# Kernel tuning notes

Hardware: AMD Instinct MI355X
Metric: run time of the kernel (lower is better)

The kernel has to match this reference:

```python
import jax, jax.numpy as jnp
import numpy as np

PHI = (1.0 + 5.0 ** 0.5) / 2.0
TWO_PI = 2.0 * np.pi
LN_EPS = 1e-5


def _complex_linear(xr, xi, Wr, Wi, br, bi):
    # (Wr + i*Wi) @ (xr + i*xi) + (br + i*bi)
    yr = xr @ Wr.T - xi @ Wi.T + br
    yi = xr @ Wi.T + xi @ Wr.T + bi
    return yr, yi


def _layernorm(x, g, b):
    m = jnp.mean(x, axis=-1, keepdims=True)
    v = jnp.mean((x - m) ** 2, axis=-1, keepdims=True)
    return (x - m) * jax.lax.rsqrt(v + LN_EPS) * g + b


def reference(w, b, ip_Wr, ip_Wi, ip_br, ip_bi, ln_g, ln_b, W_qkv, log_alpha, op_Wr, op_Wi):
    B, S, D = w.shape
    H = log_alpha.shape[0]
    Dh = D // H
    scale = jnp.sqrt(jnp.asarray(Dh, w.dtype))
    alpha = jax.nn.sigmoid(log_alpha)[None, :, None]  # (1,H,1)
    ts = jnp.arange(S, dtype=w.dtype)

    def step(carry, xs):
        hr, hi, vs = carry          # (B,D),(B,D),(B,H,Dh)
        w_t, b_t, t = xs            # (B,D),(B,D),()
        # InstrumentedEulerTransform: separated theta, complex product
        wl = 1.0 + jnp.abs(w_t)
        tphi = (t * PHI) % TWO_PI   # wrap_time_periodic
        thr = hr / wl + b_t + tphi
        thi = hi / wl + b_t + tphi
        sr, cr = jnp.sin(thr), jnp.cos(thr)
        si, ci = jnp.sin(thi), jnp.cos(thi)
        hr2 = cr * ci - sr * si
        hi2 = cr * si + sr * ci
        # InstrumentedEchoChamber.forward_step
        pr, pi_ = _complex_linear(hr2, hi2, ip_Wr, ip_Wi, ip_br, ip_bi)
        xc = _layernorm(pr + pi_, ln_g, ln_b)
        qkv = (xc @ W_qkv.T).reshape(B, 3, H, Dh)
        q, k, v = qkv[:, 0], qkv[:, 1], qkv[:, 2]
        vs2 = alpha * v + (1.0 - alpha) * vs
        gate = jax.nn.sigmoid(jnp.sum(q * k, axis=-1, keepdims=True) / scale)
        retr = (gate * vs2).reshape(B, D)
        # output_proj ComplexLinear on (retr, 0), no bias
        ore = retr @ op_Wr.T
        oim = retr @ op_Wi.T
        return (hr2, hi2, vs2), (ore, oim)

    init = (jnp.zeros((B, D), w.dtype), jnp.zeros((B, D), w.dtype),
            jnp.zeros((B, H, Dh), w.dtype))
    wT = jnp.swapaxes(w, 0, 1)  # (S,B,D)
    bT = jnp.swapaxes(b, 0, 1)
    _, (or_seq, oi_seq) = jax.lax.scan(step, init, (wT, bT, ts))
    out = jnp.stack([or_seq, oi_seq])      # (2,S,B,D)
    return jnp.swapaxes(out, 1, 2)         # (2,B,S,D)


def setup_inputs() -> dict:
    key = jax.random.key(0)
    ks = jax.random.split(key, 10)
    B, S, D, H = 8, 2048, 512, 8
    s = 0.02
    return {
        "w": jax.random.normal(ks[0], (B, S, D), jnp.float32),
        "b": jax.random.normal(ks[1], (B, S, D), jnp.float32),
        "ip_Wr": jax.random.normal(ks[2], (D, D), jnp.float32) * s,
        "ip_Wi": jax.random.normal(ks[3], (D, D), jnp.float32) * s,
        "ip_br": jax.random.normal(ks[4], (D,), jnp.float32) * s,
        "ip_bi": jax.random.normal(ks[5], (D,), jnp.float32) * s,
        "ln_g": jnp.ones((D,), jnp.float32),
        "ln_b": jnp.zeros((D,), jnp.float32),
        "W_qkv": jax.random.normal(ks[6], (3 * D, D), jnp.float32) * s,
        "log_alpha": jax.random.normal(ks[7], (H,), jnp.float32),
        "op_Wr": jax.random.normal(ks[8], (D, D), jnp.float32) * s,
        "op_Wi": jax.random.normal(ks[9], (D, D), jnp.float32) * s,
    }
```

## Files before the change

kernel.cpp:

```cpp
#include <hip/hip_runtime.h>
#include <math.h>

#define BB 8
#define SS 2048
#define DD 512
#define HH 8
#define MM (BB*SS)

#define CHK 128
#define CL  16
#define CW  48

#define RT 32
#define RW 128

typedef unsigned short u16;
typedef unsigned int   u32;
typedef float f32x4 __attribute__((ext_vector_type(4)));
typedef short s16x8 __attribute__((ext_vector_type(8)));

__device__ __forceinline__ u16 f2bf(float x){
  union { float f; unsigned u; } c; c.f = x;
  unsigned r = c.u + 0x7FFF + ((c.u >> 16) & 1);
  return (u16)(r >> 16);
}
__device__ __forceinline__ float bf2f(u16 x){
  union { unsigned u; float f; } c; c.u = ((unsigned)x) << 16;
  return c.f;
}
__device__ __forceinline__ void gload16(const u16* g, u16* l){
  __builtin_amdgcn_global_load_lds(
      (const __attribute__((address_space(1))) unsigned int*)g,
      (__attribute__((address_space(3))) unsigned int*)l, 16, 0, 0);
}

__global__ void prep_all(const float* __restrict__ ipWr, const float* __restrict__ ipWi,
                         const float* __restrict__ Wqkv,
                         const float* __restrict__ opWr, const float* __restrict__ opWi,
                         const float* __restrict__ ipbr, const float* __restrict__ ipbi,
                         const float* __restrict__ la,
                         u16* __restrict__ W1, u16* __restrict__ Wq, u16* __restrict__ W3,
                         float* __restrict__ tphi2, float* __restrict__ bc,
                         float* __restrict__ alph){
  int id = blockIdx.x*256 + threadIdx.x;
  if (id < 524288){
    int n = id >> 10, k = id & 1023;
    int d = k >> 1;
    float v = (k & 1) ? (ipWr[n*512+d] - ipWi[n*512+d])
                      : (ipWr[n*512+d] + ipWi[n*512+d]);
    W1[id] = f2bf(v);
  } else if (id < 1310720){
    int i = id - 524288;
    Wq[i] = f2bf(Wqkv[i]);
  } else if (id < 1835008){
    int i = id - 1310720;
    int n = i >> 9, k = i & 511;
    W3[i] = f2bf((n < 512) ? opWr[n*512+k] : opWi[(n-512)*512+k]);
  } else if (id < 1837056){
    int t = id - 1835008;
    const float PHI_F    = 1.61803398874989484820f;
    const float TWO_PI_F = 6.28318530717958647693f;
    tphi2[t] = 2.0f * fmodf((float)t * PHI_F, TWO_PI_F);
  } else if (id < 1837568){
    int t = id - 1837056;
    bc[t] = ipbr[t] + ipbi[t];
  } else if (id < 1837576){
    int t = id - 1837568;
    alph[t] = 1.0f/(1.0f + expf(-la[t]));
  }
}

__global__ __launch_bounds__(256) void scan_h(const float* __restrict__ w,
                                              const float* __restrict__ bb,
                                              const float* __restrict__ tphi2,
                                              u32* __restrict__ X32){
  const int e = blockIdx.x*256 + threadIdx.x;
  const int c = blockIdx.y;
  const int b = e >> 9;
  const int d = e & 511;
  const float SQRT2 = 1.41421356237309504880f;
  const float PI_4  = 0.78539816339744830962f;
  const int tstart = c*CL;
  int t0 = tstart - CW; if (t0 < 0) t0 = 0;
  const int nw = tstart - t0;

  const float* wp = w  + ((size_t)b*SS + t0)*DD + d;
  const float* bp = bb + ((size_t)b*SS + t0)*DD + d;
  const float* tp = tphi2 + t0;

  const int U = 8;
  float wv[U], bv[U], wn[U], bn[U];

  float ss = 0.f;
  const int ngw = nw >> 3;
  if (ngw > 0){
    #pragma unroll
    for (int i=0;i<U;i++){ wv[i] = wp[(size_t)i*DD]; bv[i] = bp[(size_t)i*DD]; }
    for (int gg=0; gg<ngw; ++gg){
      if (gg+1 < ngw){
        const float* wnp = wp + (size_t)(gg+1)*U*DD;
        const float* bnp = bp + (size_t)(gg+1)*U*DD;
        #pragma unroll
        for (int i=0;i<U;i++){ wn[i] = wnp[(size_t)i*DD]; bn[i] = bnp[(size_t)i*DD]; }
      }
      #pragma unroll
      for (int i=0;i<U;i++){
        float rwl2 = SQRT2 * __builtin_amdgcn_rcpf(1.0f + fabsf(wv[i]));
        float cw   = fmaf(2.0f, bv[i], tp[gg*U+i]) + PI_4;
        ss = __sinf(fmaf(ss, rwl2, cw));
      }
      #pragma unroll
      for (int i=0;i<U;i++){ wv[i]=wn[i]; bv[i]=bn[i]; }
    }
  }
  float hs = SQRT2 * ss;

  const float* wq = wp + (size_t)nw*DD;
  const float* bq = bp + (size_t)nw*DD;
  const float* tq = tp + nw;
  u32* xp = X32 + (size_t)(b*SS + tstart)*512 + d;

  #pragma unroll
  for (int i=0;i<U;i++){ wv[i] = wq[(size_t)i*DD]; bv[i] = bq[(size_t)i*DD]; }
  for (int gg=0; gg<CL/U; ++gg){
    if (gg+1 < CL/U){
      const float* wnp = wq + (size_t)(gg+1)*U*DD;
      const float* bnp = bq + (size_t)(gg+1)*U*DD;
      #pragma unroll
      for (int i=0;i<U;i++){ wn[i] = wnp[(size_t)i*DD]; bn[i] = bnp[(size_t)i*DD]; }
    }
    #pragma unroll
    for (int i=0;i<U;i++){
      float rwl = __builtin_amdgcn_rcpf(1.0f + fabsf(wv[i]));
      float cc  = fmaf(2.0f, bv[i], tq[gg*U+i]);
      float theta = fmaf(hs, rwl, cc);
      float sn = __sinf(theta);
      float cs = __cosf(theta);
      hs = cs + sn;
      xp[(size_t)(gg*U+i)*512] = (u32)f2bf(cs) | ((u32)f2bf(sn) << 16);
    }
    #pragma unroll
    for (int i=0;i<U;i++){ wv[i]=wn[i]; bv[i]=bn[i]; }
  }
}

template<int TAG, int EPI>
__global__ __launch_bounds__(256) void gemm_bf16(const u16* __restrict__ A,
                                                 const u16* __restrict__ W,
                                                 float* __restrict__ C0,
                                                 float* __restrict__ C1,
                                                 u16* __restrict__ C2,
                                                 int N, int K){
  __shared__ __align__(16) u16 As[3][128*32];
  __shared__ __align__(16) u16 Bs[3][128*32];
  const int tid  = threadIdx.x;
  const int nwgx = gridDim.x;
  const int nwg  = nwgx * gridDim.y;
  const int lin  = blockIdx.y * nwgx + blockIdx.x;
  const int qq   = nwg >> 3;
  const int logi = (lin & 7) * qq + (lin >> 3);
  const int m0   = (logi / nwgx) * 128;
  const int n0   = (logi % nwgx) * 128;

  const int wave = tid >> 6;
  const int lane = tid & 63;
  const int wr   = wave >> 1, wc = wave & 1;
  const int l15  = lane & 15;
  const int g    = lane >> 4;

  const int rI   = lane >> 2;
  const int kgs  = (lane & 3) ^ ((lane >> 3) & 3);
  const int row0 = (wave*2+0)*16 + rI;
  const int row1 = (wave*2+1)*16 + rI;
  const u16* Asrc0 = A + (size_t)(m0 + row0) * K + kgs*8;
  const u16* Asrc1 = A + (size_t)(m0 + row1) * K + kgs*8;
  const u16* Bsrc0 = W + (size_t)(n0 + row0) * K + kgs*8;
  const u16* Bsrc1 = W + (size_t)(n0 + row1) * K + kgs*8;
  const int ld0 = (wave*2+0)*512;
  const int ld1 = (wave*2+1)*512;

  f32x4 acc[4][4];
  #pragma unroll
  for (int i=0;i<4;i++)
    #pragma unroll
    for (int j=0;j<4;j++) acc[i][j] = (f32x4){0.f,0.f,0.f,0.f};

#define STAGE(buf, koff) do {                      \
    gload16(Asrc0 + (koff), &As[buf][ld0]);        \
    gload16(Asrc1 + (koff), &As[buf][ld1]);        \
    gload16(Bsrc0 + (koff), &Bs[buf][ld0]);        \
    gload16(Bsrc1 + (koff), &Bs[buf][ld1]);        \
  } while(0)

#define COMPUTE(buf) do {                                            \
    s16x8 af[4], bf[4];                                              \
    _Pragma("unroll")                                                \
    for (int s=0;s<4;s++){                                           \
      int rA = wr*64 + s*16 + l15;                                   \
      af[s] = *(const s16x8*)&As[buf][rA*32 + ((g ^ ((rA>>1)&3))*8)];\
      int rB = wc*64 + s*16 + l15;                                   \
      bf[s] = *(const s16x8*)&Bs[buf][rB*32 + ((g ^ ((rB>>1)&3))*8)];\
    }                                                                \
    _Pragma("unroll")                                                \
    for (int mi=0;mi<4;mi++)                                         \
      _Pragma("unroll")                                              \
      for (int ni=0;ni<4;ni++)                                       \
        acc[mi][ni] = __builtin_amdgcn_mfma_f32_16x16x32_bf16(af[mi], bf[ni], acc[mi][ni], 0, 0, 0); \
  } while(0)

  const int nt = K >> 5;
  STAGE(0, 0);
  STAGE(1, 32);
  int cur = 0;
  for (int t = 0; t < nt; ++t){
    if (t+2 < nt){
      int nb = cur+2; if (nb >= 3) nb -= 3;
      STAGE(nb, (t+2)*32);
      asm volatile("s_waitcnt vmcnt(8)" ::: "memory");
    } else if (t+1 < nt){
      asm volatile("s_waitcnt vmcnt(4)" ::: "memory");
    } else {
      asm volatile("s_waitcnt vmcnt(0)" ::: "memory");
    }
    __builtin_amdgcn_s_barrier();
    COMPUTE(cur);
    asm volatile("" ::: "memory");
    __builtin_amdgcn_s_barrier();
    cur = (cur==2) ? 0 : cur+1;
  }

#undef STAGE
#undef COMPUTE

  #pragma unroll
  for (int mi=0;mi<4;mi++){
    #pragma unroll
    for (int j=0;j<4;j++){
      int r = m0 + wr*64 + mi*16 + g*4 + j;
      #pragma unroll
      for (int ni=0;ni<4;ni++){
        int col = n0 + wc*64 + ni*16 + l15;
        float v = acc[mi][ni][j];
        if (EPI == 1){
          if (col < 512) C0[(size_t)r*512 + col]       = v;
          else           C1[(size_t)r*512 + (col-512)] = v;
        } else {
          C2[(size_t)r*N + col] = f2bf(v);
        }
      }
    }
  }
}

__global__ __launch_bounds__(256) void ln_kernel(const u16* __restrict__ y,
                                                 const float* __restrict__ bc,
                                                 const float* __restrict__ g,
                                                 const float* __restrict__ bb,
                                                 u16* __restrict__ xc){
  const int row  = blockIdx.x*4 + (threadIdx.x >> 6);
  const int lane = threadIdx.x & 63;
  s16x8 v = *(const s16x8*)(y + (size_t)row*512 + lane*8);
  float4 c0 = ((const float4*)bc)[lane*2];
  float4 c1 = ((const float4*)bc)[lane*2+1];
  float f[8];
  f[0] = bf2f((u16)v[0]) + c0.x; f[1] = bf2f((u16)v[1]) + c0.y;
  f[2] = bf2f((u16)v[2]) + c0.z; f[3] = bf2f((u16)v[3]) + c0.w;
  f[4] = bf2f((u16)v[4]) + c1.x; f[5] = bf2f((u16)v[5]) + c1.y;
  f[6] = bf2f((u16)v[6]) + c1.z; f[7] = bf2f((u16)v[7]) + c1.w;
  float s = 0.f, s2 = 0.f;
  #pragma unroll
  for (int i=0;i<8;i++){ s += f[i]; s2 = fmaf(f[i], f[i], s2); }
  #pragma unroll
  for (int off=32; off>0; off>>=1){ s += __shfl_xor(s, off); s2 += __shfl_xor(s2, off); }
  float mean = s * (1.0f/512.0f);
  float var  = s2 * (1.0f/512.0f) - mean*mean;
  float rstd = rsqrtf(var + 1e-5f);
  float4 g0 = ((const float4*)g)[lane*2],  g1 = ((const float4*)g)[lane*2+1];
  float4 b0 = ((const float4*)bb)[lane*2], b1 = ((const float4*)bb)[lane*2+1];
  s16x8 o;
  o[0] = (short)f2bf((f[0]-mean)*rstd*g0.x + b0.x);
  o[1] = (short)f2bf((f[1]-mean)*rstd*g0.y + b0.y);
  o[2] = (short)f2bf((f[2]-mean)*rstd*g0.z + b0.z);
  o[3] = (short)f2bf((f[3]-mean)*rstd*g0.w + b0.w);
  o[4] = (short)f2bf((f[4]-mean)*rstd*g1.x + b1.x);
  o[5] = (short)f2bf((f[5]-mean)*rstd*g1.y + b1.y);
  o[6] = (short)f2bf((f[6]-mean)*rstd*g1.z + b1.z);
  o[7] = (short)f2bf((f[7]-mean)*rstd*g1.w + b1.w);
  *(s16x8*)(xc + (size_t)row*512 + lane*8) = o;
}

__global__ __launch_bounds__(256) void retr_fused(const u16* __restrict__ qkv,
                                                  const float* __restrict__ alph,
                                                  u16* __restrict__ retr){
  const int wid  = blockIdx.x*4 + (threadIdx.x >> 6);
  const int lane = threadIdx.x & 63;
  const int c = wid & 63;
  const int h = (wid >> 6) & 7;
  const int b = wid >> 9;
  const float a  = alph[h];
  const float om = 1.0f - a;
  const int d  = h*64 + lane;
  const int t0 = c*RT;
  int w0 = t0 - RW; if (w0 < 0) w0 = 0;
  const int nw = t0 - w0;

  const u16* vp = qkv + ((size_t)(b*SS + w0))*1536 + 1024 + d;
  float vs = 0.f;
  {
    const int U = 8;
    float vv[U], vn[U];
    const int ng = nw >> 3;
    if (ng > 0){
      #pragma unroll
      for (int i=0;i<U;i++) vv[i] = bf2f(vp[(size_t)i*1536]);
      for (int gg=0; gg<ng; ++gg){
        if (gg+1 < ng){
          const u16* vnp = vp + (size_t)(gg+1)*U*1536;
          #pragma unroll
          for (int i=0;i<U;i++) vn[i] = bf2f(vnp[(size_t)i*1536]);
        }
        #pragma unroll
        for (int i=0;i<U;i++) vs = fmaf(a, vv[i], om*vs);
        #pragma unroll
        for (int i=0;i<U;i++) vv[i] = vn[i];
      }
    }
  }
  const u16* qp = qkv + ((size_t)(b*SS + t0))*1536 + d;
  u16* op = retr + ((size_t)(b*SS + t0))*512 + d;
  #pragma unroll 4
  for (int i=0;i<RT;i++){
    float q  = bf2f(qp[(size_t)i*1536]);
    float kk = bf2f(qp[(size_t)i*1536 + 512]);
    float v  = bf2f(qp[(size_t)i*1536 + 1024]);
    vs = fmaf(a, v, om*vs);
    float p = q*kk;
    #pragma unroll
    for (int off=32; off>0; off>>=1) p += __shfl_xor(p, off);
    float gate = 1.0f/(1.0f + __expf(-p*0.125f));
    op[(size_t)i*512] = f2bf(gate * vs);
  }
}

extern "C" void kernel_launch(void* const* d_in, const int* in_sizes, int n_in,
                              void* d_out, int out_size, void* d_ws, size_t ws_size,
                              hipStream_t stream) {
  const float* w    = (const float*)d_in[0];
  const float* b    = (const float*)d_in[1];
  const float* ipWr = (const float*)d_in[2];
  const float* ipWi = (const float*)d_in[3];
  const float* ipbr = (const float*)d_in[4];
  const float* ipbi = (const float*)d_in[5];
  const float* lng  = (const float*)d_in[6];
  const float* lnb  = (const float*)d_in[7];
  const float* Wqkv = (const float*)d_in[8];
  const float* la   = (const float*)d_in[9];
  const float* opWr = (const float*)d_in[10];
  const float* opWi = (const float*)d_in[11];
  float* out0 = (float*)d_out;
  float* out1 = out0 + (size_t)MM*DD;

  char* base = (char*)d_ws;
  u16*   W1    = (u16*)  (base + 0);
  u16*   Wq    = (u16*)  (base + 1048576);
  u16*   W3    = (u16*)  (base + 2621440);
  float* bc    = (float*)(base + 3670016);
  float* alph  = (float*)(base + 3672064);
  float* tphi2 = (float*)(base + 3672128);
  u32*   X32   = (u32*)  (base + 3680384);
  u16*   y     = (u16*)  (base + 37234816);
  u16*   xc    = (u16*)  (base + 54012032);
  u16*   qkv   = (u16*)  (base + 70789248);
  u16*   retr  = (u16*)X32;

  prep_all<<<7179,256,0,stream>>>(ipWr, ipWi, Wqkv, opWr, opWi, ipbr, ipbi, la,
                                  W1, Wq, W3, tphi2, bc, alph);

  scan_h<<<dim3(16,CHK),256,0,stream>>>(w, b, tphi2, X32);

  gemm_bf16<1,2><<<dim3(4,128),256,0,stream>>>((const u16*)X32, W1, nullptr, nullptr, y, 512, 1024);
  ln_kernel<<<4096,256,0,stream>>>(y, bc, lng, lnb, xc);
  gemm_bf16<2,2><<<dim3(12,128),256,0,stream>>>(xc, Wq, nullptr, nullptr, qkv, 1536, 512);

  retr_fused<<<1024,256,0,stream>>>(qkv, alph, retr);

  gemm_bf16<3,1><<<dim3(8,128),256,0,stream>>>(retr, W3, out0, out1, nullptr, 1024, 512);
}
```

Before: 159.2 us.

## Shrink GEMM tile to 64x128 with double buffering and doubled grid

Changes the bf16 MFMA GEMM from a 128x128 tile with triple-buffered LDS to a 64x128 tile with double buffering. The grid along M doubles so each GEMM launches twice as many workgroups, which is meant to improve occupancy and CU coverage on the 256-CU part and to reduce LDS per block. In exchange each block reuses less data per load, so global and LDS traffic per FLOP rises, and the prefetch depth drops from two stages to one.

Measured after the change: 169.1 us. 6.2% more time.

```diff
diff --git a/kernel.cpp b/kernel.cpp
--- a/kernel.cpp
+++ b/kernel.cpp
@@ -151,58 +151,58 @@
                                                  float* __restrict__ C1,
                                                  u16* __restrict__ C2,
                                                  int N, int K){
-  __shared__ __align__(16) u16 As[3][128*32];
-  __shared__ __align__(16) u16 Bs[3][128*32];
+  __shared__ __align__(16) u16 As[2][64*32];
+  __shared__ __align__(16) u16 Bs[2][128*32];
   const int tid  = threadIdx.x;
   const int nwgx = gridDim.x;
   const int nwg  = nwgx * gridDim.y;
   const int lin  = blockIdx.y * nwgx + blockIdx.x;
   const int qq   = nwg >> 3;
   const int logi = (lin & 7) * qq + (lin >> 3);
-  const int m0   = (logi / nwgx) * 128;
+  const int m0   = (logi / nwgx) * 64;
   const int n0   = (logi % nwgx) * 128;
 
   const int wave = tid >> 6;
   const int lane = tid & 63;
-  const int wr   = wave >> 1, wc = wave & 1;
+  const int wm   = wave >> 1;
+  const int wn   = wave & 1;
   const int l15  = lane & 15;
   const int g    = lane >> 4;
 
-  const int rI   = lane >> 2;
-  const int kgs  = (lane & 3) ^ ((lane >> 3) & 3);
-  const int row0 = (wave*2+0)*16 + rI;
-  const int row1 = (wave*2+1)*16 + rI;
-  const u16* Asrc0 = A + (size_t)(m0 + row0) * K + kgs*8;
-  const u16* Asrc1 = A + (size_t)(m0 + row1) * K + kgs*8;
-  const u16* Bsrc0 = W + (size_t)(n0 + row0) * K + kgs*8;
-  const u16* Bsrc1 = W + (size_t)(n0 + row1) * K + kgs*8;
-  const int ld0 = (wave*2+0)*512;
-  const int ld1 = (wave*2+1)*512;
-
-  f32x4 acc[4][4];
-  #pragma unroll
-  for (int i=0;i<4;i++)
+  const int kgs  = (tid & 3) ^ ((tid >> 3) & 3);
+  const u16* Asrc  = A + (size_t)(m0 + (tid>>2)) * K + kgs*8;
+  const u16* Bsrc0 = W + (size_t)(n0 + (tid>>2)) * K + kgs*8;
+  const u16* Bsrc1 = Bsrc0 + (size_t)64 * K;
+  const int dA  = tid*8;
+  const int dB0 = tid*8;
+  const int dB1 = tid*8 + 2048;
+
+  f32x4 acc[2][4];
+  #pragma unroll
+  for (int i=0;i<2;i++)
     #pragma unroll
     for (int j=0;j<4;j++) acc[i][j] = (f32x4){0.f,0.f,0.f,0.f};
 
-#define STAGE(buf, koff) do {                      \
-    gload16(Asrc0 + (koff), &As[buf][ld0]);        \
-    gload16(Asrc1 + (koff), &As[buf][ld1]);        \
-    gload16(Bsrc0 + (koff), &Bs[buf][ld0]);        \
-    gload16(Bsrc1 + (koff), &Bs[buf][ld1]);        \
+#define STAGE(buf, koff) do {                 \
+    gload16(Asrc  + (koff), &As[buf][dA]);    \
+    gload16(Bsrc0 + (koff), &Bs[buf][dB0]);   \
+    gload16(Bsrc1 + (koff), &Bs[buf][dB1]);   \
   } while(0)
 
 #define COMPUTE(buf) do {                                            \
-    s16x8 af[4], bf[4];                                              \
+    s16x8 af[2], bf[4];                                              \
+    _Pragma("unroll")                                                \
+    for (int s=0;s<2;s++){                                           \
+      int rA = wm*32 + s*16 + l15;                                   \
+      af[s] = *(const s16x8*)&As[buf][rA*32 + ((g ^ ((rA>>1)&3))*8)];\
+    }                                                                \
     _Pragma("unroll")                                                \
     for (int s=0;s<4;s++){                                           \
-      int rA = wr*64 + s*16 + l15;                                   \
-      af[s] = *(const s16x8*)&As[buf][rA*32 + ((g ^ ((rA>>1)&3))*8)];\
-      int rB = wc*64 + s*16 + l15;                                   \
+      int rB = wn*64 + s*16 + l15;                                   \
       bf[s] = *(const s16x8*)&Bs[buf][rB*32 + ((g ^ ((rB>>1)&3))*8)];\
     }                                                                \
     _Pragma("unroll")                                                \
-    for (int mi=0;mi<4;mi++)                                         \
+    for (int mi=0;mi<2;mi++)                                         \
       _Pragma("unroll")                                              \
       for (int ni=0;ni<4;ni++)                                       \
         acc[mi][ni] = __builtin_amdgcn_mfma_f32_16x16x32_bf16(af[mi], bf[ni], acc[mi][ni], 0, 0, 0); \
@@ -210,15 +210,11 @@
 
   const int nt = K >> 5;
   STAGE(0, 0);
-  STAGE(1, 32);
   int cur = 0;
   for (int t = 0; t < nt; ++t){
-    if (t+2 < nt){
-      int nb = cur+2; if (nb >= 3) nb -= 3;
-      STAGE(nb, (t+2)*32);
-      asm volatile("s_waitcnt vmcnt(8)" ::: "memory");
-    } else if (t+1 < nt){
-      asm volatile("s_waitcnt vmcnt(4)" ::: "memory");
+    if (t+1 < nt){
+      STAGE(cur^1, (t+1)*32);
+      asm volatile("s_waitcnt vmcnt(3)" ::: "memory");
     } else {
       asm volatile("s_waitcnt vmcnt(0)" ::: "memory");
     }
@@ -226,20 +222,20 @@
     COMPUTE(cur);
     asm volatile("" ::: "memory");
     __builtin_amdgcn_s_barrier();
-    cur = (cur==2) ? 0 : cur+1;
+    cur ^= 1;
   }
 
 #undef STAGE
 #undef COMPUTE
 
   #pragma unroll
-  for (int mi=0;mi<4;mi++){
+  for (int mi=0;mi<2;mi++){
     #pragma unroll
     for (int j=0;j<4;j++){
-      int r = m0 + wr*64 + mi*16 + g*4 + j;
+      int r = m0 + wm*32 + mi*16 + g*4 + j;
       #pragma unroll
       for (int ni=0;ni<4;ni++){
-        int col = n0 + wc*64 + ni*16 + l15;
+        int col = n0 + wn*64 + ni*16 + l15;
         float v = acc[mi][ni][j];
         if (EPI == 1){
           if (col < 512) C0[(size_t)r*512 + col]       = v;
@@ -378,11 +374,11 @@
 
   scan_h<<<dim3(16,CHK),256,0,stream>>>(w, b, tphi2, X32);
 
-  gemm_bf16<1,2><<<dim3(4,128),256,0,stream>>>((const u16*)X32, W1, nullptr, nullptr, y, 512, 1024);
+  gemm_bf16<1,2><<<dim3(4,256),256,0,stream>>>((const u16*)X32, W1, nullptr, nullptr, y, 512, 1024);
   ln_kernel<<<4096,256,0,stream>>>(y, bc, lng, lnb, xc);
-  gemm_bf16<2,2><<<dim3(12,128),256,0,stream>>>(xc, Wq, nullptr, nullptr, qkv, 1536, 512);
+  gemm_bf16<2,2><<<dim3(12,256),256,0,stream>>>(xc, Wq, nullptr, nullptr, qkv, 1536, 512);
 
   retr_fused<<<1024,256,0,stream>>>(qkv, alph, retr);
 
-  gemm_bf16<3,1><<<dim3(8,128),256,0,stream>>>(retr, W3, out0, out1, nullptr, 1024, 512);
-}
+  gemm_bf16<3,1><<<dim3(8,256),256,0,stream>>>(retr, W3, out0, out1, nullptr, 1024, 512);
+}
```
